# Performance work log

Measured on AMD Instinct MI355X. Metric: run time of the kernel, lower is better.

Reference implementation:

```python
import jax, jax.numpy as jnp
import numpy as np

N = 729        # problem variables
B = 8          # batch
K = 32         # mixing rank (hard-coded in MixingFunc)
NB = 40        # number of symmetry-basis matrices
MAX_ITER = 10  # coordinate-descent sweeps


def setup_inputs() -> dict:
    key = jax.random.key(0)
    ks = jax.random.split(key, 7)
    coeff = jax.random.normal(ks[0], (NB,), jnp.float32)
    upper = jax.random.normal(ks[1], (N,), jnp.float32)
    basis = jax.random.normal(ks[2], (NB, N, N), jnp.float32)
    z = jax.random.uniform(ks[3], (B, N), jnp.float32)
    is_input = jax.random.randint(ks[4], (B, N), 0, 2).astype(jnp.int32)
    v_init_raw = jax.random.normal(ks[5], (B, N + 1, K), jnp.float32)
    # random permutation of the N non-truth variables (indices 1..N), as in satnet init
    perm = (jax.random.permutation(ks[6], N) + 1).astype(jnp.int32)
    return dict(coeff=coeff, upper=upper, basis=basis, z=z,
                is_input=is_input, v_init_raw=v_init_raw, perm=perm)


def _build_C(coeff, upper, basis):
    # BasisFunc.forward: C = [[0, upper^T], [upper, sum_b coeff_b * basis_b]]
    center = jnp.einsum('b,bij->ij', coeff, basis)              # (N, N)
    top = jnp.concatenate([jnp.zeros((1,), upper.dtype), upper])[None, :]  # (1, N+1)
    bottom = jnp.concatenate([upper[:, None], center], axis=1)  # (N, N+1)
    return jnp.concatenate([top, bottom], axis=0)               # (N+1, N+1)


def _init_V(v_raw, z_full):
    # SATNet init: v0 = random unit truth direction; each v_i is placed on the
    # cone around v0 at angle pi*z_i using a random orthogonal direction.
    v0 = v_raw[:, 0] / jnp.linalg.norm(v_raw[:, 0], axis=-1, keepdims=True)  # (B, K)
    dot = jnp.einsum('bnk,bk->bn', v_raw, v0)
    u = v_raw - dot[..., None] * v0[:, None, :]
    u = u / jnp.maximum(jnp.linalg.norm(u, axis=-1, keepdims=True), 1e-8)
    c = jnp.cos(jnp.pi * z_full)[..., None]
    s = jnp.sin(jnp.pi * z_full)[..., None]
    V = -c * v0[:, None, :] + s * u                              # (B, N+1, K)
    V = V.at[:, 0].set(v0)                                       # truth vector pinned
    return V


def _mix(C, V, is_input_full, perm):
    # SATNet mixing coordinate descent: for each free variable i,
    #   g_i = sum_j C[j,i] v_j - C[i,i] v_i ;  v_i <- -g_i / ||g_i||
    Cdiag = jnp.diagonal(C)
    free = (is_input_full == 0)                                  # (B, N+1)

    def coord_step(V, i):
        g = jnp.einsum('j,bjk->bk', C[:, i], V) - Cdiag[i] * V[:, i]  # (B, K)
        gn = jnp.linalg.norm(g, axis=-1, keepdims=True)
        vnew = -g / jnp.maximum(gn, 1e-8)
        V = V.at[:, i].set(jnp.where(free[:, i][:, None], vnew, V[:, i]))
        return V, None

    def sweep(V, _):
        V, _ = jax.lax.scan(coord_step, V, perm)
        return V, None

    V, _ = jax.lax.scan(jax.checkpoint(sweep), V, None, length=MAX_ITER)
    return V


def reference(coeff, upper, basis, z, is_input, v_init_raw, perm):
    Bn = z.shape[0]
    C = _build_C(coeff, upper, basis)
    z_full = jnp.concatenate([jnp.ones((Bn, 1), z.dtype), z], axis=1)
    ii_full = jnp.concatenate(
        [jnp.ones((Bn, 1), is_input.dtype), is_input], axis=1)
    V = _init_V(v_init_raw, z_full)
    V = _mix(C, V, ii_full, perm)
    v0 = V[:, 0]
    cosang = jnp.clip(-jnp.einsum('bnk,bk->bn', V, v0), -1.0 + 1e-6, 1.0 - 1e-6)
    zo = jnp.arccos(cosang) / jnp.pi
    z_out = jnp.where(ii_full == 1, z_full, zo)
    return z_out[:, 1:]
```

## Files before the change

kernel.cpp:

```cpp
#include <hip/hip_runtime.h>

#define NN   729
#define NF   730
#define BV   8
#define KK   32
#define NBAS 40
#define MAXIT 10
#define PI_F 3.14159265358979323846f

#define MTH  512
#define BT   16
#define AST  448
#define WST  36

__device__ __forceinline__ void fma4(float4& a, float c, const float4& d) {
    a.x = fmaf(c, d.x, a.x); a.y = fmaf(c, d.y, a.y);
    a.z = fmaf(c, d.z, a.z); a.w = fmaf(c, d.w, a.w);
}

__global__ void build_C_kernel(const float* __restrict__ coeff,
                               const float* __restrict__ upper,
                               const float* __restrict__ basis,
                               float* __restrict__ Ct) {
    int idx = blockIdx.x * blockDim.x + threadIdx.x;
    if (idx >= NF * NF) return;
    int i = idx / NF, j = idx - i * NF;
    float val;
    if (i == 0) {
        val = (j == 0) ? 0.f : upper[j - 1];
    } else if (j == 0) {
        val = upper[i - 1];
    } else {
        float acc = 0.f;
        const float* bp = basis + (size_t)(i - 1) * NN + (j - 1);
        #pragma unroll 8
        for (int b = 0; b < NBAS; ++b)
            acc = fmaf(coeff[b], bp[(size_t)b * NN * NN], acc);
        val = acc;
    }
    Ct[(size_t)j * NF + i] = val;
}

__global__ void init_V_kernel(const float* __restrict__ z,
                              const float* __restrict__ vraw,
                              float* __restrict__ V) {
    int g = threadIdx.x >> 5;
    int k = threadIdx.x & 31;
    int row = blockIdx.x * 8 + g;
    int b = row / NF, n = row - b * NF;
    const float* vr = vraw + (size_t)b * NF * KK;

    float v0 = vr[k];
    float s2 = v0 * v0;
    #pragma unroll
    for (int off = 16; off; off >>= 1) s2 += __shfl_xor(s2, off, 32);
    v0 = v0 / sqrtf(s2);

    float vn = vr[(size_t)n * KK + k];
    float d = vn * v0;
    #pragma unroll
    for (int off = 16; off; off >>= 1) d += __shfl_xor(d, off, 32);
    float u = vn - d * v0;
    float un2 = u * u;
    #pragma unroll
    for (int off = 16; off; off >>= 1) un2 += __shfl_xor(un2, off, 32);
    u = u / fmaxf(sqrtf(un2), 1e-8f);

    float zf = (n == 0) ? 1.f : z[b * NN + (n - 1)];
    float c = cosf(PI_F * zf), s = sinf(PI_F * zf);
    float outv = -c * v0 + s * u;
    if (n == 0) outv = v0;
    V[((size_t)b * NF + n) * KK + k] = outv;
}

__global__ void build_act_kernel(const int* __restrict__ is_input,
                                 const int* __restrict__ perm,
                                 int* __restrict__ act, int* __restrict__ nA_arr) {
    int b = blockIdx.x, l = threadIdx.x;
    int base = 0;
    for (int c = 0; c < (NN + 63) / 64; ++c) {
        int idx = c * 64 + l;
        bool f = false; int pi = 0;
        if (idx < NN) { pi = perm[idx]; f = (is_input[b * NN + pi - 1] == 0); }
        unsigned long long m = __ballot(f);
        int pos = __popcll(m & ((1ull << l) - 1ull));
        if (f && base + pos < AST) act[b * AST + base + pos] = pi;
        base += __popcll(m);
    }
    if (base > AST) base = AST;
    if (l == 0) nA_arr[b] = base;
    for (int p = base + l; p < AST; p += 64) act[b * AST + p] = 0;
}

__global__ void gather_CactT_kernel(const float* __restrict__ Ct,
                                    const int* __restrict__ act,
                                    float* __restrict__ CactT) {
    int a = blockIdx.x, b = blockIdx.y;
    __shared__ int acts[AST];
    for (int i = threadIdx.x; i < AST; i += blockDim.x) acts[i] = act[b * AST + i];
    __syncthreads();
    const float* src = Ct + (size_t)acts[a] * NF;
    float* dst = CactT + ((size_t)b * AST + a) * AST;
    for (int t = threadIdx.x; t < AST; t += blockDim.x)
        dst[t] = src[acts[t]];
}

__global__ void init_W_kernel(const float* __restrict__ Ct,
                              const int* __restrict__ act,
                              const int* __restrict__ nA_arr,
                              const float* __restrict__ V,
                              float* __restrict__ Wc) {
    int b = blockIdx.y;
    int a = blockIdx.x * 8 + (threadIdx.x >> 5);
    int k = threadIdx.x & 31;
    int nA = nA_arr[b];
    float w = 0.f;
    if (a < nA) {
        int ra = act[b * AST + a];
        const float* ctr = Ct + (size_t)ra * NF;
        const float* vb = V + (size_t)b * NF * KK + k;
        float acc = 0.f;
        for (int j = 0; j < NF; ++j)
            acc = fmaf(ctr[j], vb[(size_t)j * KK], acc);
        float cd = ctr[ra];
        w = acc - cd * V[((size_t)b * NF + ra) * KK + k];
    }
    Wc[((size_t)b * AST + a) * KK + k] = w;
}

__device__ __forceinline__ float rowsum16(float x) {
    int y;
    y = __builtin_amdgcn_update_dpp(0, __float_as_int(x), 0x121, 0xF, 0xF, false);
    x += __int_as_float(y);
    y = __builtin_amdgcn_update_dpp(0, __float_as_int(x), 0x122, 0xF, 0xF, false);
    x += __int_as_float(y);
    y = __builtin_amdgcn_update_dpp(0, __float_as_int(x), 0x124, 0xF, 0xF, false);
    x += __int_as_float(y);
    y = __builtin_amdgcn_update_dpp(0, __float_as_int(x), 0x128, 0xF, 0xF, false);
    x += __int_as_float(y);
    return x;
}

__global__ __launch_bounds__(MTH, 2)
void mix_kernel(const float* __restrict__ CactT_g,
                const float* __restrict__ Wc,
                const int* __restrict__ act_g,
                const int* __restrict__ nA_arr,
                const int* __restrict__ is_input,
                const float* __restrict__ z,
                const float* __restrict__ Vg,
                float* __restrict__ out) {
    __shared__ float W_c[AST * WST];
    __shared__ float V_c[AST * KK];
    __shared__ float dv_s[2][BT * KK];
    __shared__ float cblk_s[2][BT * BT];
    __shared__ int   act_s[AST];
    __shared__ int   slot_s[NF];

    int b = blockIdx.x, tid = threadIdx.x;
    const float* CactT_b = CactT_g + (size_t)b * AST * AST;
    int nA = nA_arr[b];
    int nblkp = (nA + BT - 1) / BT;
    if (nblkp < 2) nblkp = 2;
    int nAp = nblkp * BT;
    int totB = MAXIT * nblkp;

    if (tid < AST) act_s[tid] = act_g[b * AST + tid];
    __syncthreads();
    for (int idx = tid; idx < nAp * KK; idx += MTH) {
        int a = idx >> 5, k = idx & 31;
        V_c[idx] = Vg[((size_t)b * NF + act_s[a]) * KK + k];
        W_c[a * WST + k] = Wc[((size_t)b * AST + a) * KK + k];
    }
    if (tid < nA) slot_s[act_s[tid]] = tid;
    if (tid < BT * BT)
        cblk_s[0][tid] = CactT_b[(size_t)(tid & 15) * AST + (tid >> 4)];
    __syncthreads();

    int wid = tid >> 6;
    int laneb = tid - 64;
    int k4b = (laneb & 7) * 4;
    int ar = laneb >> 3;

    float4 pfc[4];
    float4 cp[4][4];
    if (wid > 0) {
        #pragma unroll
        for (int mm = 0; mm < 4; ++mm)
            #pragma unroll
            for (int j = 0; j < 4; ++j)
                cp[mm][j] = *(const float4*)&CactT_b[(size_t)(ar + 56 * mm) * AST + 4 * j];
    }

    for (int bi = 0; bi < totB; ++bi) {
        int blk = bi % nblkp;
        int s0 = blk * BT;
        int pblk = (bi - 1) % nblkp;
        int sp0 = pblk * BT;
        int cb = bi & 1, pv = cb ^ 1;

        if (wid == 0) {
            int u4 = tid >> 2, kq = (tid & 3) * 8;
            if (bi > 0) {
                float4 wA = *(float4*)&W_c[(s0 + u4) * WST + kq];
                float4 wB = *(float4*)&W_c[(s0 + u4) * WST + kq + 4];
                #pragma unroll
                for (int j = 0; j < 4; ++j) {
                    float4 cj = pfc[j];
                    float4 dA, dB;
                    dA = *(float4*)&dv_s[pv][(4*j+0) * KK + kq];
                    dB = *(float4*)&dv_s[pv][(4*j+0) * KK + kq + 4];
                    fma4(wA, cj.x, dA); fma4(wB, cj.x, dB);
                    dA = *(float4*)&dv_s[pv][(4*j+1) * KK + kq];
                    dB = *(float4*)&dv_s[pv][(4*j+1) * KK + kq + 4];
                    fma4(wA, cj.y, dA); fma4(wB, cj.y, dB);
                    dA = *(float4*)&dv_s[pv][(4*j+2) * KK + kq];
                    dB = *(float4*)&dv_s[pv][(4*j+2) * KK + kq + 4];
                    fma4(wA, cj.z, dA); fma4(wB, cj.z, dB);
                    dA = *(float4*)&dv_s[pv][(4*j+3) * KK + kq];
                    dB = *(float4*)&dv_s[pv][(4*j+3) * KK + kq + 4];
                    fma4(wA, cj.w, dA); fma4(wB, cj.w, dB);
                }
                *(float4*)&W_c[(s0 + u4) * WST + kq] = wA;
                *(float4*)&W_c[(s0 + u4) * WST + kq + 4] = wB;
            }
            {
                int s0n = ((bi + 1) % nblkp) * BT;
                #pragma unroll
                for (int j = 0; j < 4; ++j)
                    pfc[j] = *(const float4*)&CactT_b[(size_t)(s0n + u4) * AST + s0 + 4 * j];
            }
            __builtin_amdgcn_wave_barrier();

            int ll = tid & 15;
            float g0[BT], g1[BT];
            #pragma unroll
            for (int u = 0; u < BT; ++u) {
                g0[u] = W_c[(s0 + u) * WST + ll];
                g1[u] = W_c[(s0 + u) * WST + ll + 16];
            }
            #pragma unroll
            for (int u = 0; u < BT; ++u) {
                int s = s0 + u;
                float n2 = fmaf(g0[u], g0[u], g1[u] * g1[u]);
                n2 = rowsum16(n2);
                float inv = -__builtin_amdgcn_rsqf(fmaxf(n2, 1e-16f));
                float vo0 = V_c[s * KK + ll];
                float vo1 = V_c[s * KK + ll + 16];
                float msk = (s < nA) ? 1.f : 0.f;
                float d0 = fmaf(g0[u], inv, -vo0) * msk;
                float d1 = fmaf(g1[u], inv, -vo1) * msk;
                if (tid < 16) {
                    dv_s[cb][u * KK + ll]      = d0;
                    dv_s[cb][u * KK + ll + 16] = d1;
                    V_c[s * KK + ll]      = vo0 + d0;
                    V_c[s * KK + ll + 16] = vo1 + d1;
                }
                #pragma unroll
                for (int u2 = u + 1; u2 < BT; ++u2) {
                    float c = cblk_s[cb][u * BT + u2];
                    g0[u2] = fmaf(c, d0, g0[u2]);
                    g1[u2] = fmaf(c, d1, g1[u2]);
                }
            }
        } else {
            if (wid == 7) {
                int sn0 = ((bi + 1) % nblkp) * BT;
                int l = tid & 63;
                #pragma unroll
                for (int qq = 0; qq < 4; ++qq) {
                    int idx = qq * 64 + l;
                    cblk_s[pv][idx] =
                        CactT_b[(size_t)(sn0 + (idx & 15)) * AST + sn0 + (idx >> 4)];
                }
            }
            if (bi > 0) {
                float4 dvv[BT];
                #pragma unroll
                for (int t = 0; t < BT; ++t)
                    dvv[t] = *(float4*)&dv_s[pv][t * KK + k4b];
                #pragma unroll
                for (int mm = 0; mm < 8; ++mm) {
                    int a = ar + 56 * mm;
                    int mb = mm & 3;
                    if (a < nAp && (a >> 4) != blk) {
                        float4 w = *(float4*)&W_c[a * WST + k4b];
                        #pragma unroll
                        for (int j = 0; j < 4; ++j) {
                            float4 cj = cp[mb][j];
                            fma4(w, cj.x, dvv[4*j+0]);
                            fma4(w, cj.y, dvv[4*j+1]);
                            fma4(w, cj.z, dvv[4*j+2]);
                            fma4(w, cj.w, dvv[4*j+3]);
                        }
                        if ((a >> 4) == pblk) {
                            float cd = -CactT_b[(size_t)a * AST + a];
                            float4 dd = *(float4*)&dv_s[pv][(a - sp0) * KK + k4b];
                            fma4(w, cd, dd);
                        }
                        *(float4*)&W_c[a * WST + k4b] = w;
                    }
                    {
                        int col = (mm < 4) ? sp0 : s0;
                        int an  = (mm < 4) ? (a + 224) : (ar + 56 * (mm - 4));
                        #pragma unroll
                        for (int j = 0; j < 4; ++j)
                            cp[mb][j] = *(const float4*)&CactT_b[(size_t)an * AST + col + 4 * j];
                    }
                }
            }
        }
        __syncthreads();
    }

    int k = tid & 31, r = tid >> 5;
    float v0k = Vg[(size_t)b * NF * KK + k];
    for (int n = 1 + r; n <= NN; n += 16) {
        int ii = is_input[b * NN + n - 1];
        float res;
        if (ii == 1) {
            res = z[b * NN + n - 1];
        } else {
            int a = slot_s[n];
            float dot = V_c[a * KK + k] * v0k;
            #pragma unroll
            for (int off = 16; off; off >>= 1) dot += __shfl_xor(dot, off, 32);
            float ca = fminf(fmaxf(-dot, -1.f + 1e-6f), 1.f - 1e-6f);
            res = acosf(ca) * (1.f / PI_F);
        }
        if (k == 0) out[b * NN + n - 1] = res;
    }
}

extern "C" void kernel_launch(void* const* d_in, const int* in_sizes, int n_in,
                              void* d_out, int out_size, void* d_ws, size_t ws_size,
                              hipStream_t stream) {
    const float* coeff    = (const float*)d_in[0];
    const float* upper    = (const float*)d_in[1];
    const float* basis    = (const float*)d_in[2];
    const float* z        = (const float*)d_in[3];
    const int*   is_input = (const int*)d_in[4];
    const float* vraw     = (const float*)d_in[5];
    const int*   perm     = (const int*)d_in[6];
    float* out = (float*)d_out;

    float* ws    = (float*)d_ws;
    float* Ct    = ws;
    float* V     = Ct + (size_t)NF * NF;
    float* CactT = V + (size_t)BV * NF * KK;
    float* Wc    = CactT + (size_t)BV * AST * AST;
    int*   act   = (int*)(Wc + (size_t)BV * AST * KK);
    int*   nAa   = act + BV * AST;

    build_C_kernel<<<dim3((NF * NF + 255) / 256), dim3(256), 0, stream>>>(coeff, upper, basis, Ct);
    init_V_kernel<<<dim3(730), dim3(256), 0, stream>>>(z, vraw, V);
    build_act_kernel<<<dim3(BV), dim3(64), 0, stream>>>(is_input, perm, act, nAa);
    gather_CactT_kernel<<<dim3(AST, BV), dim3(256), 0, stream>>>(Ct, act, CactT);
    init_W_kernel<<<dim3(AST / 8, BV), dim3(256), 0, stream>>>(Ct, act, nAa, V, Wc);
    mix_kernel<<<dim3(BV), dim3(MTH), 0, stream>>>(CactT, Wc, act, nAa, is_input, z, V, out);
}
```

Baseline: 787.0 us.

## Keep accumulated gradients in registers across 1024 threads with per-block publish

The block grows from 512 to 1024 threads. Each bulk thread now keeps its share of the gradient accumulators W in registers (8 rows by 2 k-values) instead of in a shared W_c array. The rows of the current block are brought up to date with a small C mini-block and published to shared memory for the serial wave, which costs an extra __syncthreads per block step. C rows are prefetched two passes ahead, and the diagonal is cached in shared memory. The intent is to spread the rank-16 update over more waves and drop the shared-memory round trips for W, at the cost of an extra barrier and fewer registers per thread.

```diff
diff --git a/kernel.cpp b/kernel.cpp
--- a/kernel.cpp
+++ b/kernel.cpp
@@ -8,14 +8,18 @@
 #define MAXIT 10
 #define PI_F 3.14159265358979323846f
 
-#define MTH  512
-#define BT   16
-#define AST  448
-#define WST  36
-
-__device__ __forceinline__ void fma4(float4& a, float c, const float4& d) {
-    a.x = fmaf(c, d.x, a.x); a.y = fmaf(c, d.y, a.y);
-    a.z = fmaf(c, d.z, a.z); a.w = fmaf(c, d.w, a.w);
+#define MTH   1024
+#define BT    16
+#define AST   448
+#define NSLOT 60
+#define NPASS 8
+
+typedef float v2f __attribute__((ext_vector_type(2)));
+
+__device__ __forceinline__ v2f fma2(float c, v2f d, v2f w) {
+    w.x = fmaf(c, d.x, w.x);
+    w.y = fmaf(c, d.y, w.y);
+    return w;
 }
 
 __global__ void build_C_kernel(const float* __restrict__ coeff,
@@ -141,7 +145,7 @@
     return x;
 }
 
-__global__ __launch_bounds__(MTH, 2)
+__global__ __launch_bounds__(MTH)
 void mix_kernel(const float* __restrict__ CactT_g,
                 const float* __restrict__ Wc,
                 const int* __restrict__ act_g,
@@ -150,10 +154,12 @@
                 const float* __restrict__ z,
                 const float* __restrict__ Vg,
                 float* __restrict__ out) {
-    __shared__ float W_c[AST * WST];
     __shared__ float V_c[AST * KK];
+    __shared__ float gpub[BT * KK];
     __shared__ float dv_s[2][BT * KK];
     __shared__ float cblk_s[2][BT * BT];
+    __shared__ float cmini_s[2][BT * BT];
+    __shared__ float Cd_s[AST];
     __shared__ int   act_s[AST];
     __shared__ int   slot_s[NF];
 
@@ -165,79 +171,66 @@
     int nAp = nblkp * BT;
     int totB = MAXIT * nblkp;
 
+    int wid = tid >> 6;
+    bool isbulk = (tid >= 64);
+    int lane = isbulk ? (tid - 64) : 0;
+    int kp = lane & 15;
+    int slot = lane >> 4;
+
     if (tid < AST) act_s[tid] = act_g[b * AST + tid];
     __syncthreads();
-    for (int idx = tid; idx < nAp * KK; idx += MTH) {
-        int a = idx >> 5, k = idx & 31;
-        V_c[idx] = Vg[((size_t)b * NF + act_s[a]) * KK + k];
-        W_c[a * WST + k] = Wc[((size_t)b * AST + a) * KK + k];
-    }
+    for (int idx = tid; idx < nAp * KK; idx += MTH)
+        V_c[idx] = Vg[((size_t)b * NF + act_s[idx >> 5]) * KK + (idx & 31)];
     if (tid < nA) slot_s[act_s[tid]] = tid;
-    if (tid < BT * BT)
-        cblk_s[0][tid] = CactT_b[(size_t)(tid & 15) * AST + (tid >> 4)];
+    if (tid < AST) Cd_s[tid] = CactT_b[(size_t)tid * AST + tid];
+    if (tid < 256) {
+        int t = tid >> 4, u = tid & 15;
+        cblk_s[0][t * BT + u] = CactT_b[(size_t)u * AST + t];
+    }
+    v2f w[NPASS];
+    #pragma unroll
+    for (int p = 0; p < NPASS; ++p) {
+        int a = slot + NSLOT * p;
+        v2f zz = {0.f, 0.f};
+        w[p] = zz;
+        if (isbulk && a < AST)
+            w[p] = *(const v2f*)&Wc[((size_t)b * AST + a) * KK + 2 * kp];
+    }
     __syncthreads();
 
-    int wid = tid >> 6;
-    int laneb = tid - 64;
-    int k4b = (laneb & 7) * 4;
-    int ar = laneb >> 3;
-
-    float4 pfc[4];
-    float4 cp[4][4];
-    if (wid > 0) {
-        #pragma unroll
-        for (int mm = 0; mm < 4; ++mm)
+    for (int bi = 0; bi < totB; ++bi) {
+        int blk = bi % nblkp, s0 = blk * BT;
+        int pblk = (bi - 1 + nblkp) % nblkp, sp0 = pblk * BT;
+        int cb = bi & 1, pv = cb ^ 1;
+        int sn0 = ((bi + 1) % nblkp) * BT;
+
+        if (isbulk) {
             #pragma unroll
-            for (int j = 0; j < 4; ++j)
-                cp[mm][j] = *(const float4*)&CactT_b[(size_t)(ar + 56 * mm) * AST + 4 * j];
-    }
-
-    for (int bi = 0; bi < totB; ++bi) {
-        int blk = bi % nblkp;
-        int s0 = blk * BT;
-        int pblk = (bi - 1) % nblkp;
-        int sp0 = pblk * BT;
-        int cb = bi & 1, pv = cb ^ 1;
+            for (int p = 0; p < NPASS; ++p) {
+                int a = slot + NSLOT * p;
+                if ((a >> 4) == blk) {
+                    int u = a - s0;
+                    if (bi > 0) {
+                        #pragma unroll
+                        for (int t = 0; t < BT; ++t) {
+                            float c = cmini_s[cb][u * BT + t];
+                            v2f d = *(const v2f*)&dv_s[pv][t * KK + 2 * kp];
+                            w[p] = fma2(c, d, w[p]);
+                        }
+                    }
+                    *(v2f*)&gpub[u * KK + 2 * kp] = w[p];
+                }
+            }
+        }
+        __syncthreads();
 
         if (wid == 0) {
-            int u4 = tid >> 2, kq = (tid & 3) * 8;
-            if (bi > 0) {
-                float4 wA = *(float4*)&W_c[(s0 + u4) * WST + kq];
-                float4 wB = *(float4*)&W_c[(s0 + u4) * WST + kq + 4];
-                #pragma unroll
-                for (int j = 0; j < 4; ++j) {
-                    float4 cj = pfc[j];
-                    float4 dA, dB;
-                    dA = *(float4*)&dv_s[pv][(4*j+0) * KK + kq];
-                    dB = *(float4*)&dv_s[pv][(4*j+0) * KK + kq + 4];
-                    fma4(wA, cj.x, dA); fma4(wB, cj.x, dB);
-                    dA = *(float4*)&dv_s[pv][(4*j+1) * KK + kq];
-                    dB = *(float4*)&dv_s[pv][(4*j+1) * KK + kq + 4];
-                    fma4(wA, cj.y, dA); fma4(wB, cj.y, dB);
-                    dA = *(float4*)&dv_s[pv][(4*j+2) * KK + kq];
-                    dB = *(float4*)&dv_s[pv][(4*j+2) * KK + kq + 4];
-                    fma4(wA, cj.z, dA); fma4(wB, cj.z, dB);
-                    dA = *(float4*)&dv_s[pv][(4*j+3) * KK + kq];
-                    dB = *(float4*)&dv_s[pv][(4*j+3) * KK + kq + 4];
-                    fma4(wA, cj.w, dA); fma4(wB, cj.w, dB);
-                }
-                *(float4*)&W_c[(s0 + u4) * WST + kq] = wA;
-                *(float4*)&W_c[(s0 + u4) * WST + kq + 4] = wB;
-            }
-            {
-                int s0n = ((bi + 1) % nblkp) * BT;
-                #pragma unroll
-                for (int j = 0; j < 4; ++j)
-                    pfc[j] = *(const float4*)&CactT_b[(size_t)(s0n + u4) * AST + s0 + 4 * j];
-            }
-            __builtin_amdgcn_wave_barrier();
-
             int ll = tid & 15;
             float g0[BT], g1[BT];
             #pragma unroll
             for (int u = 0; u < BT; ++u) {
-                g0[u] = W_c[(s0 + u) * WST + ll];
-                g1[u] = W_c[(s0 + u) * WST + ll + 16];
+                g0[u] = gpub[u * KK + ll];
+                g1[u] = gpub[u * KK + ll + 16];
             }
             #pragma unroll
             for (int u = 0; u < BT; ++u) {
@@ -264,48 +257,79 @@
                 }
             }
         } else {
-            if (wid == 7) {
-                int sn0 = ((bi + 1) % nblkp) * BT;
-                int l = tid & 63;
-                #pragma unroll
-                for (int qq = 0; qq < 4; ++qq) {
-                    int idx = qq * 64 + l;
-                    cblk_s[pv][idx] =
-                        CactT_b[(size_t)(sn0 + (idx & 15)) * AST + sn0 + (idx >> 4)];
-                }
+            if (wid == 14) {
+                int l = tid & 63; int u = l & 15, q = l >> 4;
+                float4 v = *(const float4*)&CactT_b[(size_t)(sn0 + u) * AST + s0 + 4 * q];
+                *(float4*)&cmini_s[pv][u * BT + 4 * q] = v;
+            }
+            if (wid == 15) {
+                int l = tid & 63; int u = l & 15, q = l >> 4;
+                float4 v = *(const float4*)&CactT_b[(size_t)(sn0 + u) * AST + sn0 + 4 * q];
+                cblk_s[pv][(4 * q + 0) * BT + u] = v.x;
+                cblk_s[pv][(4 * q + 1) * BT + u] = v.y;
+                cblk_s[pv][(4 * q + 2) * BT + u] = v.z;
+                cblk_s[pv][(4 * q + 3) * BT + u] = v.w;
             }
             if (bi > 0) {
-                float4 dvv[BT];
+                v2f dvv[BT];
                 #pragma unroll
                 for (int t = 0; t < BT; ++t)
-                    dvv[t] = *(float4*)&dv_s[pv][t * KK + k4b];
+                    dvv[t] = *(const v2f*)&dv_s[pv][t * KK + 2 * kp];
+                const float* cbase = CactT_b + sp0;
+                float4 cbA[4], cbB[4];
+                {
+                    const float* r0 = cbase + (size_t)slot * AST;
+                    const float* r1 = cbase + (size_t)(slot + NSLOT) * AST;
+                    cbA[0] = *(const float4*)(r0);      cbB[0] = *(const float4*)(r1);
+                    cbA[1] = *(const float4*)(r0 + 4);  cbB[1] = *(const float4*)(r1 + 4);
+                    cbA[2] = *(const float4*)(r0 + 8);  cbB[2] = *(const float4*)(r1 + 8);
+                    cbA[3] = *(const float4*)(r0 + 12); cbB[3] = *(const float4*)(r1 + 12);
+                }
                 #pragma unroll
-                for (int mm = 0; mm < 8; ++mm) {
-                    int a = ar + 56 * mm;
-                    int mb = mm & 3;
+                for (int p = 0; p < NPASS; ++p) {
+                    float4 q0 = (p & 1) ? cbB[0] : cbA[0];
+                    float4 q1 = (p & 1) ? cbB[1] : cbA[1];
+                    float4 q2 = (p & 1) ? cbB[2] : cbA[2];
+                    float4 q3 = (p & 1) ? cbB[3] : cbA[3];
+                    int a = slot + NSLOT * p;
+                    if (p < NPASS - 2) {
+                        int an = slot + NSLOT * (p + 2);
+                        if (an < AST) {
+                            const float* rn = cbase + (size_t)an * AST;
+                            if (p & 1) {
+                                cbB[0] = *(const float4*)(rn);
+                                cbB[1] = *(const float4*)(rn + 4);
+                                cbB[2] = *(const float4*)(rn + 8);
+                                cbB[3] = *(const float4*)(rn + 12);
+                            } else {
+                                cbA[0] = *(const float4*)(rn);
+                                cbA[1] = *(const float4*)(rn + 4);
+                                cbA[2] = *(const float4*)(rn + 8);
+                                cbA[3] = *(const float4*)(rn + 12);
+                            }
+                        }
+                    }
                     if (a < nAp && (a >> 4) != blk) {
-                        float4 w = *(float4*)&W_c[a * WST + k4b];
-                        #pragma unroll
-                        for (int j = 0; j < 4; ++j) {
-                            float4 cj = cp[mb][j];
-                            fma4(w, cj.x, dvv[4*j+0]);
-                            fma4(w, cj.y, dvv[4*j+1]);
-                            fma4(w, cj.z, dvv[4*j+2]);
-                            fma4(w, cj.w, dvv[4*j+3]);
+                        w[p] = fma2(q0.x, dvv[0],  w[p]);
+                        w[p] = fma2(q0.y, dvv[1],  w[p]);
+                        w[p] = fma2(q0.z, dvv[2],  w[p]);
+                        w[p] = fma2(q0.w, dvv[3],  w[p]);
+                        w[p] = fma2(q1.x, dvv[4],  w[p]);
+                        w[p] = fma2(q1.y, dvv[5],  w[p]);
+                        w[p] = fma2(q1.z, dvv[6],  w[p]);
+                        w[p] = fma2(q1.w, dvv[7],  w[p]);
+                        w[p] = fma2(q2.x, dvv[8],  w[p]);
+                        w[p] = fma2(q2.y, dvv[9],  w[p]);
+                        w[p] = fma2(q2.z, dvv[10], w[p]);
+                        w[p] = fma2(q2.w, dvv[11], w[p]);
+                        w[p] = fma2(q3.x, dvv[12], w[p]);
+                        w[p] = fma2(q3.y, dvv[13], w[p]);
+                        w[p] = fma2(q3.z, dvv[14], w[p]);
+                        w[p] = fma2(q3.w, dvv[15], w[p]);
+                        if ((a >> 4) == pblk) {
+                            v2f dd = *(const v2f*)&dv_s[pv][(a - sp0) * KK + 2 * kp];
+                            w[p] = fma2(-Cd_s[a], dd, w[p]);
                         }
-                        if ((a >> 4) == pblk) {
-                            float cd = -CactT_b[(size_t)a * AST + a];
-                            float4 dd = *(float4*)&dv_s[pv][(a - sp0) * KK + k4b];
-                            fma4(w, cd, dd);
-                        }
-                        *(float4*)&W_c[a * WST + k4b] = w;
-                    }
-                    {
-                        int col = (mm < 4) ? sp0 : s0;
-                        int an  = (mm < 4) ? (a + 224) : (ar + 56 * (mm - 4));
-                        #pragma unroll
-                        for (int j = 0; j < 4; ++j)
-                            cp[mb][j] = *(const float4*)&CactT_b[(size_t)an * AST + col + 4 * j];
                     }
                 }
             }
@@ -315,7 +339,7 @@
 
     int k = tid & 31, r = tid >> 5;
     float v0k = Vg[(size_t)b * NF * KK + k];
-    for (int n = 1 + r; n <= NN; n += 16) {
+    for (int n = 1 + r; n <= NN; n += 32) {
         int ii = is_input[b * NN + n - 1];
         float res;
         if (ii == 1) {
```

Result: slower. 1.562 ms (+98.5%).
